# Performance work log

Measured on AMD Instinct MI355X. Metric: run time of the kernel, lower is better.

Reference implementation:

```python
import jax, jax.numpy as jnp
import numpy as np
import math

D_K = 8  # = n_wires; one input value encoded per wire


def setup_inputs() -> dict:
    key = jax.random.key(0)
    k1, k2, k3, k4 = jax.random.split(key, 4)
    B, S, E = 4, 2048, 1024
    x = jax.random.normal(k1, (B, S, E), dtype=jnp.float32)
    theta = jax.random.normal(k2, (D_K,), dtype=jnp.float32)  # shared RX params (one ModuleList reused per head)
    W = jax.random.normal(k3, (E, E), dtype=jnp.float32) * (1.0 / math.sqrt(E))
    b = jax.random.normal(k4, (E,), dtype=jnp.float32) * 0.01
    return {"x": x, "theta": theta, "W": W, "b": b}


def reference(x, theta, W, b):
    B, S, E = x.shape
    dk = theta.shape[0]
    H = E // dk
    # Quantum circuit collapse: RX(x_i) then RX(theta_i) on |0>, measure PauliZ
    # on each wire of a product state -> <Z_i> = cos(x_i + theta_i).
    proj = x.reshape(B, S, H, dk)
    q_out = jnp.cos(proj + theta)  # theta broadcast over (B,S,H)
    # NOTE: faithful to original — attention is over the HEAD axis: (B,S,H,H)
    attn = jnp.einsum('bshd,bsgd->bshg', q_out, q_out) / math.sqrt(dk)
    attn = jax.nn.softmax(attn, axis=-1)  # dropout is identity at inference
    out = jnp.einsum('bshg,bsgd->bshd', attn, q_out)  # (B,S,H,dk)
    # faithful transpose(1,2).contiguous().view(B,S,E) reinterleave
    out = jnp.transpose(out, (0, 2, 1, 3)).reshape(B, S, E)
    return out @ W.T + b
```

## Files before the change

### kernel.cpp

```cpp
#include <hip/hip_runtime.h>
#include <hip/hip_bf16.h>
#include <stdint.h>

typedef __attribute__((ext_vector_type(8))) short bf16x8;
typedef __attribute__((ext_vector_type(4))) float f32x4;
typedef __attribute__((ext_vector_type(16))) float f32x16;
typedef __attribute__((ext_vector_type(2))) unsigned int uint32x2;
typedef __attribute__((address_space(3))) void lds_t;
typedef __attribute__((address_space(1))) void glb_t;

#define B_ 4
#define S_ 2048
#define E_ 1024
#define M_ (B_*S_)

static __device__ __forceinline__ ushort f2bf(float f) {
  uint32_t u = __float_as_uint(f);
  u += 0x7fffu + ((u >> 16) & 1u);
  return (ushort)(u >> 16);
}

static __device__ __forceinline__ uint32_t pk_bf16(float lo, float hi) {
  uint32_t r;
  asm("v_cvt_pk_bf16_f32 %0, %1, %2" : "=v"(r) : "v"(lo), "v"(hi));
  return r;
}
static __device__ __forceinline__ float fexp2(float x) {
  float r;
  asm("v_exp_f32 %0, %1" : "=v"(r) : "v"(x));
  return r;
}

static __device__ __forceinline__ void half_zip(uint32_t a, uint32_t b, bool convA,
                                                uint32_t& X, uint32_t& Y) {
  if (convA) {
    uint32x2 r = __builtin_amdgcn_permlane32_swap(b, a, false, false);
    Y = r[0]; X = r[1];
  } else {
    uint32x2 r = __builtin_amdgcn_permlane32_swap(a, b, false, false);
    X = r[0]; Y = r[1];
  }
}

__global__ __launch_bounds__(256) void qattn(const float* __restrict__ x,
                                             const float* __restrict__ theta,
                                             ushort* __restrict__ outr) {
  const int wave = threadIdx.x >> 6;
  const int lane = threadIdx.x & 63;
  const int bs = blockIdx.x;
  const int b = bs >> 11, s = bs & 2047;
  const int l31 = lane & 31, hw = lane >> 5;

  __shared__ __align__(16) ushort qL[4][129 * 8];
  __shared__ __align__(16) ushort qT[4][16 * 144];
  ushort* qp = qL[wave];
  ushort* qt = qT[wave];

  uint32x2 pr = __builtin_amdgcn_permlane32_swap((uint32_t)lane, (uint32_t)(lane + 1000),
                                                 false, false);
  const bool convA = (__builtin_amdgcn_readfirstlane((int)pr[0]) >= 1000);

  float th[8];
  #pragma unroll
  for (int d = 0; d < 8; ++d) th[d] = theta[d];

  const float* xp = x + (size_t)bs * E_ + lane * 16;
  float xr[16];
  #pragma unroll
  for (int i = 0; i < 4; ++i) {
    const float4 v = ((const float4*)xp)[i];
    xr[4*i+0] = v.x; xr[4*i+1] = v.y; xr[4*i+2] = v.z; xr[4*i+3] = v.w;
  }
  float q0[8], q1[8];
  #pragma unroll
  for (int d = 0; d < 8; ++d) {
    q0[d] = __cosf(xr[d] + th[d]);
    q1[d] = __cosf(xr[8 + d] + th[d]);
  }

  const float QS = 0.71419165f;
  uint32_t qw[8];
  #pragma unroll
  for (int i = 0; i < 4; ++i) {
    qw[i]     = pk_bf16(q0[2*i] * QS, q0[2*i+1] * QS);
    qw[4 + i] = pk_bf16(q1[2*i] * QS, q1[2*i+1] * QS);
  }
  *(uint4*)(qp + (2*lane)     * 8) = *(uint4*)&qw[0];
  *(uint4*)(qp + (2*lane + 1) * 8) = *(uint4*)&qw[4];
  if (lane == 0) *(uint4*)(qp + 128 * 8) = make_uint4(0, 0, 0, 0);

  #pragma unroll
  for (int d = 0; d < 8; ++d)
    *(uint32_t*)(qt + d * 144 + 2 * lane) = pk_bf16(q0[d], q1[d]);
  *(uint32_t*)(qt + 8 * 144 + 2 * lane) = 0x3F803F80u;
  #pragma unroll
  for (int r = 9; r < 16; ++r)
    *(uint32_t*)(qt + r * 144 + 2 * lane) = (r == 12) ? 0x3F803F80u : 0u;

  bf16x8 qtf[8];
  const bf16x8 zf = {};
  #pragma unroll
  for (int ks = 0; ks < 8; ++ks) {
    bf16x8 f = *(const bf16x8*)(qt + (l31 & 15) * 144 + ks * 16 + hw * 8);
    qtf[ks] = (l31 < 16) ? f : zf;
  }

  const int hi = wave;
  const int brow = (lane < 32) ? (hi * 32 + l31) : 128;
  const bf16x8 bq = *(const bf16x8*)(qp + brow * 8);

  f32x16 oacc = {};

  #pragma unroll
  for (int gj = 0; gj < 4; ++gj) {
    const int arow = (lane < 32) ? (gj * 32 + l31) : 128;
    const bf16x8 aq = *(const bf16x8*)(qp + arow * 8);
    f32x16 sc = {};
    sc = __builtin_amdgcn_mfma_f32_32x32x16_bf16(aq, bq, sc, 0, 0, 0);
    float p[16];
    #pragma unroll
    for (int i = 0; i < 16; ++i) p[i] = fexp2(sc[i]);
    #pragma unroll
    for (int sl = 0; sl < 2; ++sl) {
      const int pb = sl * 8;
      const uint32_t u = pk_bf16(p[pb+0], p[pb+1]);
      const uint32_t v = pk_bf16(p[pb+2], p[pb+3]);
      const uint32_t w = pk_bf16(p[pb+4], p[pb+5]);
      const uint32_t z = pk_bf16(p[pb+6], p[pb+7]);
      uint32_t f0, f1, f2, f3;
      half_zip(u, w, convA, f0, f2);
      half_zip(v, z, convA, f1, f3);
      uint32_t fr[4] = {f0, f1, f2, f3};
      oacc = __builtin_amdgcn_mfma_f32_32x32x16_bf16(qtf[gj*2 + sl], *(const bf16x8*)fr,
                                                     oacc, 0, 0, 0);
    }
  }

  const int scol = s & 127, srow = s >> 7;
  const float inv = __builtin_amdgcn_rcpf(oacc[4]);
  const uint32_t o01 = pk_bf16(oacc[0] * inv, oacc[1] * inv);
  const uint32_t o23 = pk_bf16(oacc[2] * inv, oacc[3] * inv);
  const int h = hi * 32 + l31;
  const size_t row = (size_t)(b * 2048 + h * 16 + srow);
  *(uint2*)(outr + row * E_ + scol * 8 + hw * 4) = make_uint2(o01, o23);
}

__global__ __launch_bounds__(256) void wconv(const float* __restrict__ W,
                                             ushort* __restrict__ Wb) {
  const int i = blockIdx.x * 256 + threadIdx.x;
  const float4 v = ((const float4*)W)[i];
  ushort4 o;
  o.x = f2bf(v.x); o.y = f2bf(v.y); o.z = f2bf(v.z); o.w = f2bf(v.w);
  ((ushort4*)Wb)[i] = o;
}

__global__ __launch_bounds__(256) void gemm_bt(const ushort* __restrict__ A,
                                               const ushort* __restrict__ Bw,
                                               const float* __restrict__ bias,
                                               float* __restrict__ C) {
  __shared__ __align__(16) ushort As[128 * 32];
  __shared__ __align__(16) ushort Bs[128 * 32];

  const int t = threadIdx.x;
  const int lane = t & 63;
  const int wavei = t >> 6;
  const int wr = wavei >> 1, wc = wavei & 1;
  const int lhi = lane >> 4, llo = lane & 15;
  const size_t ar0 = (size_t)blockIdx.x * 128;
  const size_t br0 = (size_t)blockIdx.y * 128;

  const int c0 = t, c1 = t + 256;
  const int r0 = c0 >> 2, kp0 = (c0 & 3) * 8;
  const int r1 = c1 >> 2, kp1 = (c1 & 3) * 8;

  f32x4 acc[4][4] = {};

  for (int k0 = 0; k0 < E_; k0 += 32) {
    __builtin_amdgcn_global_load_lds((const glb_t*)(A  + (ar0 + r0) * E_ + k0 + kp0),
                                     (lds_t*)(As + c0 * 8), 16, 0, 0);
    __builtin_amdgcn_global_load_lds((const glb_t*)(A  + (ar0 + r1) * E_ + k0 + kp1),
                                     (lds_t*)(As + c1 * 8), 16, 0, 0);
    __builtin_amdgcn_global_load_lds((const glb_t*)(Bw + (br0 + r0) * E_ + k0 + kp0),
                                     (lds_t*)(Bs + c0 * 8), 16, 0, 0);
    __builtin_amdgcn_global_load_lds((const glb_t*)(Bw + (br0 + r1) * E_ + k0 + kp1),
                                     (lds_t*)(Bs + c1 * 8), 16, 0, 0);
    __syncthreads();

    bf16x8 af[4], bfr[4];
    #pragma unroll
    for (int i = 0; i < 4; ++i)
      af[i] = *(const bf16x8*)(As + (wr * 64 + i * 16 + llo) * 32 + lhi * 8);
    #pragma unroll
    for (int j = 0; j < 4; ++j)
      bfr[j] = *(const bf16x8*)(Bs + (wc * 64 + j * 16 + llo) * 32 + lhi * 8);

    #pragma unroll
    for (int i = 0; i < 4; ++i)
      #pragma unroll
      for (int j = 0; j < 4; ++j)
        acc[i][j] = __builtin_amdgcn_mfma_f32_16x16x32_bf16(af[i], bfr[j], acc[i][j], 0, 0, 0);

    __syncthreads();
  }

  #pragma unroll
  for (int j = 0; j < 4; ++j) {
    const int n = (int)br0 + wc * 64 + j * 16 + llo;
    const float bj = bias[n];
    #pragma unroll
    for (int i = 0; i < 4; ++i) {
      const int mb = (int)ar0 + wr * 64 + i * 16 + lhi * 4;
      #pragma unroll
      for (int r = 0; r < 4; ++r) {
        C[(size_t)(mb + r) * E_ + n] = acc[i][j][r] + bj;
      }
    }
  }
}

extern "C" void kernel_launch(void* const* d_in, const int* in_sizes, int n_in,
                              void* d_out, int out_size, void* d_ws, size_t ws_size,
                              hipStream_t stream) {
  const float* x     = (const float*)d_in[0];
  const float* theta = (const float*)d_in[1];
  const float* W     = (const float*)d_in[2];
  const float* bias  = (const float*)d_in[3];
  float* out = (float*)d_out;

  ushort* outr = (ushort*)d_ws;
  ushort* Wb   = (ushort*)((char*)d_ws + (size_t)M_ * E_ * 2);

  qattn<<<M_, 256, 0, stream>>>(x, theta, outr);
  wconv<<<(E_ * E_) / (256 * 4), 256, 0, stream>>>(W, Wb);
  dim3 g(M_ / 128, E_ / 128);
  gemm_bt<<<g, 256, 0, stream>>>(outr, Wb, bias, out);
}
```

Before: 75.99 us.

## Share q tiles across waves in LDS and remap block-to-row order

Previously every wave redundantly loaded the full 1024-element x row, computed all 1024 cosines and wrote its own private copy of the q tiles in LDS. Now the four waves split that work, each thread handling 4 elements, write a single shared LDS copy, and synchronize with a block barrier. Block indices are also permuted so consecutive blocks map to rows strided across batch and sequence, which changes output write locality. The aim is to cut the 4x redundant global loads, cosines and LDS traffic, at the cost of a __syncthreads and scalar 16-bit transposed LDS stores that may bank-conflict.

```diff
diff --git a/kernel.cpp b/kernel.cpp
--- a/kernel.cpp
+++ b/kernel.cpp
@@ -47,55 +47,45 @@
                                              ushort* __restrict__ outr) {
   const int wave = threadIdx.x >> 6;
   const int lane = threadIdx.x & 63;
-  const int bs = blockIdx.x;
+  const int bid = blockIdx.x;
+  const int bs = (bid & 7) * 1024 + (bid >> 3);
   const int b = bs >> 11, s = bs & 2047;
   const int l31 = lane & 31, hw = lane >> 5;
 
-  __shared__ __align__(16) ushort qL[4][129 * 8];
-  __shared__ __align__(16) ushort qT[4][16 * 144];
-  ushort* qp = qL[wave];
-  ushort* qt = qT[wave];
+  __shared__ __align__(16) ushort qp[129 * 8];
+  __shared__ __align__(16) ushort qt[16 * 144];
 
   uint32x2 pr = __builtin_amdgcn_permlane32_swap((uint32_t)lane, (uint32_t)(lane + 1000),
                                                  false, false);
   const bool convA = (__builtin_amdgcn_readfirstlane((int)pr[0]) >= 1000);
 
-  float th[8];
-  #pragma unroll
-  for (int d = 0; d < 8; ++d) th[d] = theta[d];
-
-  const float* xp = x + (size_t)bs * E_ + lane * 16;
-  float xr[16];
-  #pragma unroll
-  for (int i = 0; i < 4; ++i) {
-    const float4 v = ((const float4*)xp)[i];
-    xr[4*i+0] = v.x; xr[4*i+1] = v.y; xr[4*i+2] = v.z; xr[4*i+3] = v.w;
-  }
-  float q0[8], q1[8];
-  #pragma unroll
-  for (int d = 0; d < 8; ++d) {
-    q0[d] = __cosf(xr[d] + th[d]);
-    q1[d] = __cosf(xr[8 + d] + th[d]);
-  }
-
-  const float QS = 0.71419165f;
-  uint32_t qw[8];
-  #pragma unroll
-  for (int i = 0; i < 4; ++i) {
-    qw[i]     = pk_bf16(q0[2*i] * QS, q0[2*i+1] * QS);
-    qw[4 + i] = pk_bf16(q1[2*i] * QS, q1[2*i+1] * QS);
-  }
-  *(uint4*)(qp + (2*lane)     * 8) = *(uint4*)&qw[0];
-  *(uint4*)(qp + (2*lane + 1) * 8) = *(uint4*)&qw[4];
-  if (lane == 0) *(uint4*)(qp + 128 * 8) = make_uint4(0, 0, 0, 0);
-
-  #pragma unroll
-  for (int d = 0; d < 8; ++d)
-    *(uint32_t*)(qt + d * 144 + 2 * lane) = pk_bf16(q0[d], q1[d]);
-  *(uint32_t*)(qt + 8 * 144 + 2 * lane) = 0x3F803F80u;
-  #pragma unroll
-  for (int r = 9; r < 16; ++r)
-    *(uint32_t*)(qt + r * 144 + 2 * lane) = (r == 12) ? 0x3F803F80u : 0u;
+  {
+    const int h  = 32 * wave + (lane >> 1);
+    const int dh = (lane & 1) * 4;
+    const float4 xv = *(const float4*)(x + (size_t)bs * E_ + h * 8 + dh);
+    float q[4];
+    q[0] = __cosf(xv.x + theta[dh + 0]);
+    q[1] = __cosf(xv.y + theta[dh + 1]);
+    q[2] = __cosf(xv.z + theta[dh + 2]);
+    q[3] = __cosf(xv.w + theta[dh + 3]);
+
+    const float QS = 0.71419165f;
+    uint2 pw;
+    pw.x = pk_bf16(q[0] * QS, q[1] * QS);
+    pw.y = pk_bf16(q[2] * QS, q[3] * QS);
+    *(uint2*)(qp + h * 8 + dh) = pw;
+
+    #pragma unroll
+    for (int j = 0; j < 4; ++j)
+      qt[(dh + j) * 144 + h] = f2bf(q[j]);
+    #pragma unroll
+    for (int j = 0; j < 4; ++j)
+      qt[(8 + dh + j) * 144 + h] = (j == 0) ? (ushort)0x3F80u : (ushort)0u;
+
+    if (lane == 0) *(uint4*)(qp + 128 * 8) = make_uint4(0, 0, 0, 0);
+  }
+  __syncthreads();
+  __builtin_amdgcn_sched_barrier(0);
 
   bf16x8 qtf[8];
   const bf16x8 zf = {};
```

New measurement: 69.27 us. 8.8% less time.
